# Kernel optimization log

Hardware: AMD Instinct MI355X
Metric: run time of the kernel (lower is better)

The kernel has to match this reference:

```python
import jax, jax.numpy as jnp
import numpy as np
from jax import lax

N_USERS, N_ITEMS = 40000, 60000
N = N_USERS + N_ITEMS
D = 64
E = 800000
L = 2
BIAS = 1e-4
AUTO_T = 1.0


def setup_inputs() -> dict:
    key = jax.random.key(0)
    ks = jax.random.split(key, 12)
    emb0 = jax.random.normal(ks[0], (N, D), dtype=jnp.float32) * 0.1
    h_idx = jax.random.randint(ks[1], (E,), 0, N)
    t_idx = jax.random.randint(ks[2], (E,), 0, N)
    # symmetric normalization G = D^-1/2 A D^-1/2 (values share A's sparsity)
    deg = jax.ops.segment_sum(jnp.ones((E,), jnp.float32), h_idx, num_segments=N)
    dis = jnp.where(deg > 0, deg ** -0.5, 0.0)
    G_values = dis[h_idx] * dis[t_idx]
    # Gumbel noise: -log(-log(U(bias, 1-bias)))
    ue = jax.random.uniform(ks[3], (L, E), minval=BIAS, maxval=1.0 - BIAS)
    edge_gumbel = -jnp.log(-jnp.log(ue))
    un = jax.random.uniform(ks[4], (L, N, D), minval=BIAS, maxval=1.0 - BIAS)
    emb_gumbel = -jnp.log(-jnp.log(un))
    sc2, sc1 = (2.0 / (3 * D)) ** 0.5, (2.0 / (2 * D)) ** 0.5
    edge_W1 = jax.random.normal(ks[5], (L, 2 * D, D), dtype=jnp.float32) * sc2
    edge_b1 = jnp.zeros((L, D), jnp.float32)
    edge_W2 = jax.random.normal(ks[6], (L, D, 1), dtype=jnp.float32) * sc1
    edge_b2 = jnp.zeros((L, 1), jnp.float32)
    emb_W1 = jax.random.normal(ks[7], (L, D, D), dtype=jnp.float32) * sc1
    emb_b1 = jnp.zeros((L, D), jnp.float32)
    emb_W2 = jax.random.normal(ks[8], (L, D, D), dtype=jnp.float32) * sc1
    emb_b2 = jnp.zeros((L, D), jnp.float32)
    return dict(emb0=emb0, h_idx=h_idx, t_idx=t_idx, G_values=G_values,
                edge_gumbel=edge_gumbel, emb_gumbel=emb_gumbel,
                edge_W1=edge_W1, edge_b1=edge_b1, edge_W2=edge_W2, edge_b2=edge_b2,
                emb_W1=emb_W1, emb_b1=emb_b1, emb_W2=emb_W2, emb_b2=emb_b2)


def _spmm(vals, h, t, x, n):
    # out[h] += vals * x[t]
    return jax.ops.segment_sum(vals[:, None] * x[t], h, num_segments=n)


def reference(emb0, h_idx, t_idx, G_values, edge_gumbel, emb_gumbel,
              edge_W1, edge_b1, edge_W2, edge_b2,
              emb_W1, emb_b1, emb_W2, emb_b2):
    n = emb0.shape[0]
    e0 = e1 = e2 = emb0
    s0 = s1 = s2 = emb0
    for i in range(edge_W1.shape[0]):
        # branch 0: plain normalized propagation
        gnn0 = _spmm(G_values, h_idx, t_idx, e0, n)
        # branch 1: learned edge reweighting (auto_augment_s, is_norm=True)
        edge_emb = jnp.concatenate([e1[h_idx], e1[t_idx]], axis=1)      # [E, 2D]
        logits = jnp.maximum(edge_emb @ edge_W1[i] + edge_b1[i], 0.0) @ edge_W2[i] + edge_b2[i]  # [E,1]
        w = jax.nn.sigmoid((edge_gumbel[i][:, None] + logits) / AUTO_T)[:, 0]
        w = lax.stop_gradient(w)                                         # detached in original
        row = jax.ops.segment_sum(w, h_idx, num_segments=n)
        dinv = jnp.where(row > 0, 1.0 / row, 0.0)                        # pow(-1).nan_to_num(0)
        vals1 = dinv[h_idx] * w
        gnn1 = _spmm(vals1, h_idx, t_idx, e1, n)
        # branch 2: learned feature gating (auto_augment_f)
        lg = jnp.maximum(e2 @ emb_W1[i] + emb_b1[i], 0.0) @ emb_W2[i] + emb_b2[i]
        gate = lax.stop_gradient(jax.nn.sigmoid((emb_gumbel[i] + lg) / AUTO_T))
        gnn2 = _spmm(G_values, h_idx, t_idx, gate * e2, n)
        e0 = gnn0 + e0
        e1 = gnn1 + e1
        e2 = gnn2 + e2
        s0 = s0 + e0
        s1 = s1 + e1
        s2 = s2 + e2
    return jnp.stack([s0, s1, s2])  # [3, N, D]; split rows into users/items downstream
```

## Files before the change

### kernel.cpp

```cpp
#include <hip/hip_runtime.h>
#include <hip/hip_bf16.h>
#include <math.h>

#define PK_STRIDE 256
#define LDA 72

typedef float v4f __attribute__((ext_vector_type(4)));
typedef __attribute__((ext_vector_type(8))) short s8;
typedef __attribute__((ext_vector_type(4))) float f4;

__device__ __forceinline__ float4 f4z() { return make_float4(0.f, 0.f, 0.f, 0.f); }
__device__ __forceinline__ void fma4(float4& a, float s, const float4& v) {
  a.x = fmaf(s, v.x, a.x); a.y = fmaf(s, v.y, a.y);
  a.z = fmaf(s, v.z, a.z); a.w = fmaf(s, v.w, a.w);
}
__device__ __forceinline__ float4 add4(const float4& a, const float4& b) {
  return make_float4(a.x + b.x, a.y + b.y, a.z + b.z, a.w + b.w);
}
__device__ __forceinline__ void stnt4(float* p, const float4& v) {
  v4f u; u.x = v.x; u.y = v.y; u.z = v.z; u.w = v.w;
  __builtin_nontemporal_store(u, (v4f*)p);
}
__device__ __forceinline__ float4 lo4(const uint4& u) {
  float4 f;
  f.x = __uint_as_float(u.x << 16);
  f.y = __uint_as_float(u.x & 0xffff0000u);
  f.z = __uint_as_float(u.y << 16);
  f.w = __uint_as_float(u.y & 0xffff0000u);
  return f;
}
__device__ __forceinline__ float4 hi4(const uint4& u) {
  float4 f;
  f.x = __uint_as_float(u.z << 16);
  f.y = __uint_as_float(u.z & 0xffff0000u);
  f.z = __uint_as_float(u.w << 16);
  f.w = __uint_as_float(u.w & 0xffff0000u);
  return f;
}
__device__ __forceinline__ float4 cvt2(const uint2& u) {
  float4 f;
  f.x = __uint_as_float(u.x << 16);
  f.y = __uint_as_float(u.x & 0xffff0000u);
  f.z = __uint_as_float(u.y << 16);
  f.w = __uint_as_float(u.y & 0xffff0000u);
  return f;
}
__device__ __forceinline__ float4 ldbf4(const unsigned short* p) {
  ushort4 u = *(const ushort4*)p;
  float4 f;
  f.x = __uint_as_float((unsigned)u.x << 16);
  f.y = __uint_as_float((unsigned)u.y << 16);
  f.z = __uint_as_float((unsigned)u.z << 16);
  f.w = __uint_as_float((unsigned)u.w << 16);
  return f;
}
__device__ __forceinline__ unsigned short f2bf(float v) {
  __hip_bfloat16 h = __float2bfloat16(v);
  return *reinterpret_cast<unsigned short*>(&h);
}
__device__ __forceinline__ unsigned pack2(float a, float b) {
  return ((unsigned)f2bf(b) << 16) | (unsigned)f2bf(a);
}
__device__ __forceinline__ void st4bf(unsigned short* p, const float4& v) {
  ushort4 u;
  u.x = f2bf(v.x); u.y = f2bf(v.y); u.z = f2bf(v.z); u.w = f2bf(v.w);
  *(ushort4*)p = u;
}
__device__ __forceinline__ float fsig(float x) {
  return __builtin_amdgcn_rcpf(1.f + __expf(-x));
}

__global__ void hist_k(const int* __restrict__ h, int* __restrict__ deg, int E) {
  int i = blockIdx.x * blockDim.x + threadIdx.x;
  if (i < E) atomicAdd(&deg[h[i]], 1);
}

__global__ void scanA_k(const int* __restrict__ deg, int* __restrict__ rp,
                        int* __restrict__ sums, int N) {
  __shared__ int s[1024];
  int i = blockIdx.x * 1024 + threadIdx.x;
  int v = (i < N) ? deg[i] : 0;
  s[threadIdx.x] = v;
  __syncthreads();
  for (int off = 1; off < 1024; off <<= 1) {
    int t = (threadIdx.x >= (unsigned)off) ? s[threadIdx.x - off] : 0;
    __syncthreads();
    s[threadIdx.x] += t;
    __syncthreads();
  }
  if (i < N) rp[i] = s[threadIdx.x] - v;
  if (threadIdx.x == 1023) sums[blockIdx.x] = s[1023];
}

__global__ void scanB_k(int* sums, int nch) {
  int lane = threadIdx.x;
  int run = 0;
  for (int base = 0; base < nch; base += 64) {
    int v = (base + lane < nch) ? sums[base + lane] : 0;
    int incl = v;
    for (int off = 1; off < 64; off <<= 1) {
      int t = __shfl_up(incl, off, 64);
      if (lane >= off) incl += t;
    }
    if (base + lane < nch) sums[base + lane] = run + (incl - v);
    run += __shfl(incl, 63, 64);
  }
}

__global__ void scanC_k(int* __restrict__ rp, int* __restrict__ cur,
                        const int* __restrict__ sums, int N, int E) {
  int i = blockIdx.x * blockDim.x + threadIdx.x;
  if (i < N) {
    int v = rp[i] + sums[i >> 10];
    rp[i] = v; cur[i] = v;
  } else if (i == N) {
    rp[N] = E;
  }
}

__global__ void fill_k(const int* __restrict__ h, const int* __restrict__ t_idx,
                       const float* __restrict__ G, const float* __restrict__ gum,
                       int* __restrict__ cur, int4* __restrict__ emeta,
                       float* __restrict__ cgum, int E, int L) {
  int i = blockIdx.x * blockDim.x + threadIdx.x;
  if (i < E) {
    int pos = atomicAdd(&cur[h[i]], 1);
    int4 em;
    em.x = t_idx[i] * PK_STRIDE;
    em.y = __float_as_int(G[i]);
    em.z = __float_as_int(gum[i]);
    em.w = (L > 1) ? __float_as_int(gum[(size_t)E + i]) : 0;
    emeta[pos] = em;
    if (L > 2)
      for (int l = 2; l < L; l++) cgum[(size_t)l * E + pos] = gum[(size_t)l * E + i];
  }
}

__global__ void wprep_k(const float* __restrict__ edge_W1,
                        const float* __restrict__ emb_W1,
                        const float* __restrict__ emb_W2,
                        unsigned short* __restrict__ wxT,
                        unsigned short* __restrict__ w1T,
                        unsigned short* __restrict__ w2T, int L) {
  const int per = 128 * 64 + 64 * 64 + 64 * 64;
  int i = blockIdx.x * blockDim.x + threadIdx.x;
  if (i >= L * per) return;
  int layer = i / per, r = i % per;
  if (r < 8192) {
    int j = r >> 6, k = r & 63;
    float v = (j < 64) ? edge_W1[((size_t)layer * 128 + k) * 64 + j]
                       : edge_W1[((size_t)layer * 128 + 64 + k) * 64 + (j - 64)];
    wxT[(size_t)layer * 8192 + j * 64 + k] = f2bf(v);
  } else if (r < 8192 + 4096) {
    int q = r - 8192; int n = q >> 6, k = q & 63;
    w1T[(size_t)layer * 4096 + n * 64 + k] =
        f2bf(emb_W1[((size_t)layer * 64 + k) * 64 + n]);
  } else {
    int q = r - 12288; int n = q >> 6, k = q & 63;
    w2T[(size_t)layer * 4096 + n * 64 + k] =
        f2bf(emb_W2[((size_t)layer * 64 + k) * 64 + n]);
  }
}

template <int FIRST>
__global__ __launch_bounds__(256) void dense_k(
    const float* __restrict__ emb0,
    const unsigned short* __restrict__ pkin,
    const unsigned short* __restrict__ e2b,
    const unsigned short* __restrict__ wxT,
    const unsigned short* __restrict__ w1T,
    const unsigned short* __restrict__ w2T,
    const float* __restrict__ b1,
    const float* __restrict__ b2,
    const float* __restrict__ gum,
    unsigned short* __restrict__ xhb,
    unsigned short* __restrict__ pk,
    unsigned short* __restrict__ emb0b,
    int N) {
  __shared__ unsigned short a1[64 * LDA];
  __shared__ unsigned short a2[64 * LDA];
  int tid = threadIdx.x;
  int n0 = blockIdx.x * 64;
  if (FIRST) {
    for (int i = tid; i < 64 * 8; i += 256) {
      int r = i >> 3, c8 = (i & 7) * 8;
      uint4 u = make_uint4(0, 0, 0, 0);
      if (n0 + r < N) {
        const float* src = emb0 + (size_t)(n0 + r) * 64 + c8;
        float4 lo = *(const float4*)src;
        float4 hi = *(const float4*)(src + 4);
        u.x = pack2(lo.x, lo.y); u.y = pack2(lo.z, lo.w);
        u.z = pack2(hi.x, hi.y); u.w = pack2(hi.z, hi.w);
        *(uint4*)(emb0b + (size_t)(n0 + r) * 64 + c8) = u;
      }
      *(uint4*)(a1 + r * LDA + c8) = u;
      *(uint4*)(a2 + r * LDA + c8) = u;
    }
  } else {
    for (int i = tid; i < 64 * 16; i += 256) {
      int r = i >> 4, c = i & 15;
      ushort4 v1 = make_ushort4(0, 0, 0, 0), v2 = v1;
      if (n0 + r < N) {
        v1 = *(const ushort4*)(pkin + (size_t)(n0 + r) * PK_STRIDE + c * 8 + 4);
        v2 = *(const ushort4*)(e2b + (size_t)(n0 + r) * 64 + c * 4);
      }
      *(ushort4*)(a1 + r * LDA + c * 4) = v1;
      *(ushort4*)(a2 + r * LDA + c * 4) = v2;
    }
  }
  __syncthreads();
  int wv = tid >> 6, l = tid & 63;
  int l15 = l & 15, lg = l >> 4;
  int wr = wv * 16;
  int arow = wr + l15;
  s8 af1_0 = *(const s8*)(a1 + arow * LDA + 8 * lg);
  s8 af1_1 = *(const s8*)(a1 + arow * LDA + 32 + 8 * lg);
#pragma unroll
  for (int ct = 0; ct < 8; ct++) {
    f4 acc = {0.f, 0.f, 0.f, 0.f};
    s8 b0 = *(const s8*)(wxT + (ct * 16 + l15) * 64 + 8 * lg);
    s8 bI = *(const s8*)(wxT + (ct * 16 + l15) * 64 + 32 + 8 * lg);
    acc = __builtin_amdgcn_mfma_f32_16x16x32_bf16(af1_0, b0, acc, 0, 0, 0);
    acc = __builtin_amdgcn_mfma_f32_16x16x32_bf16(af1_1, bI, acc, 0, 0, 0);
#pragma unroll
    for (int j = 0; j < 4; j++) {
      int n = n0 + wr + lg * 4 + j;
      if (n < N) {
        if (ct < 4) {
          xhb[(size_t)n * 64 + ct * 16 + l15] = f2bf(acc[j]);
        } else {
          int c2 = (ct - 4) * 16 + l15;
          pk[(size_t)n * PK_STRIDE + 128 + (c2 >> 2) * 8 + 4 + (c2 & 3)] = f2bf(acc[j]);
        }
      }
    }
  }
  s8 af2_0 = *(const s8*)(a2 + arow * LDA + 8 * lg);
  s8 af2_1 = *(const s8*)(a2 + arow * LDA + 32 + 8 * lg);
#pragma unroll
  for (int ct = 0; ct < 4; ct++) {
    f4 acc = {0.f, 0.f, 0.f, 0.f};
    s8 b0 = *(const s8*)(w1T + (ct * 16 + l15) * 64 + 8 * lg);
    s8 bI = *(const s8*)(w1T + (ct * 16 + l15) * 64 + 32 + 8 * lg);
    acc = __builtin_amdgcn_mfma_f32_16x16x32_bf16(af2_0, b0, acc, 0, 0, 0);
    acc = __builtin_amdgcn_mfma_f32_16x16x32_bf16(af2_1, bI, acc, 0, 0, 0);
    float bb = b1[ct * 16 + l15];
#pragma unroll
    for (int j = 0; j < 4; j++) {
      float h = fmaxf(acc[j] + bb, 0.f);
      a1[(wr + lg * 4 + j) * LDA + ct * 16 + l15] = f2bf(h);
    }
  }
  s8 afh_0 = *(const s8*)(a1 + arow * LDA + 8 * lg);
  s8 afh_1 = *(const s8*)(a1 + arow * LDA + 32 + 8 * lg);
#pragma unroll
  for (int ct = 0; ct < 4; ct++) {
    f4 acc = {0.f, 0.f, 0.f, 0.f};
    s8 b0 = *(const s8*)(w2T + (ct * 16 + l15) * 64 + 8 * lg);
    s8 bI = *(const s8*)(w2T + (ct * 16 + l15) * 64 + 32 + 8 * lg);
    acc = __builtin_amdgcn_mfma_f32_16x16x32_bf16(afh_0, b0, acc, 0, 0, 0);
    acc = __builtin_amdgcn_mfma_f32_16x16x32_bf16(afh_1, bI, acc, 0, 0, 0);
    int c2 = ct * 16 + l15;
    float bb = b2[c2];
#pragma unroll
    for (int j = 0; j < 4; j++) {
      int row = wr + lg * 4 + j;
      int n = n0 + row;
      if (n < N) {
        float gv = gum[(size_t)n * 64 + c2];
        float e2v = __uint_as_float((unsigned)a2[row * LDA + c2] << 16);
        float y = e2v * fsig(gv + acc[j] + bb);
        pk[(size_t)n * PK_STRIDE + 128 + (c2 >> 2) * 8 + (c2 & 3)] = f2bf(y);
      }
    }
  }
}

#define CH 2

#define LOADCH(Abuf, Bbuf, I0)                                          \
  _Pragma("unroll")                                                     \
  for (int c = 0; c < CH; c++) {                                        \
    int i_ = (I0) + c;                                                  \
    int tof_ = __shfl(em.x, i_ & 15, 16);                               \
    if (i_ < cnt) {                                                     \
      const unsigned short* pr_ = pk + (size_t)tof_ + l * 8;            \
      Abuf[c] = *(const uint4*)(pr_);                                   \
      Bbuf[c] = *(const uint4*)(pr_ + 128);                             \
    }                                                                   \
  }

#define COMPCH(Abuf, Bbuf, I0)                                          \
  _Pragma("unroll")                                                     \
  for (int c = 0; c < CH; c++) {                                        \
    int i_ = (I0) + c;                                                  \
    float gg_ = __shfl(__int_as_float(em.y), i_ & 15, 16);              \
    float gu_ = __shfl(guv, i_ & 15, 16);                               \
    if (i_ < cnt) {                                                     \
      float4 v0_ = lo4(Abuf[c]);                                        \
      float4 v1_ = hi4(Abuf[c]);                                        \
      float4 vy_ = lo4(Bbuf[c]);                                        \
      float4 xt_ = hi4(Bbuf[c]);                                        \
      float pq_ = fmaxf(xb1.x + xt_.x, 0.f) * w2v.x                     \
                + fmaxf(xb1.y + xt_.y, 0.f) * w2v.y                     \
                + fmaxf(xb1.z + xt_.z, 0.f) * w2v.z                     \
                + fmaxf(xb1.w + xt_.w, 0.f) * w2v.w;                    \
      pq_ += __shfl_xor(pq_, 1, 16);                                    \
      pq_ += __shfl_xor(pq_, 2, 16);                                    \
      pq_ += __shfl_xor(pq_, 4, 16);                                    \
      pq_ += __shfl_xor(pq_, 8, 16);                                    \
      float w_ = fsig(gu_ + pq_ + b2s);                                 \
      wsum += w_;                                                       \
      fma4(acc0, gg_, v0_);                                             \
      fma4(acc1, w_, v1_);                                              \
      fma4(acc2, gg_, vy_);                                             \
    }                                                                   \
  }

#define LOADCH_F(Abuf, Bbuf, I0)                                        \
  _Pragma("unroll")                                                     \
  for (int c = 0; c < CH; c++) {                                        \
    int i_ = (I0) + c;                                                  \
    int tof_ = __shfl(em.x, i_ & 15, 16);                               \
    if (i_ < cnt) {                                                     \
      Abuf[c] = *(const uint2*)(emb0b + (size_t)(tof_ >> 2) + l * 4);   \
      Bbuf[c] = *(const uint4*)(pk + (size_t)tof_ + 128 + l * 8);       \
    }                                                                   \
  }

#define COMPCH_F(Abuf, Bbuf, I0)                                        \
  _Pragma("unroll")                                                     \
  for (int c = 0; c < CH; c++) {                                        \
    int i_ = (I0) + c;                                                  \
    float gg_ = __shfl(__int_as_float(em.y), i_ & 15, 16);              \
    float gu_ = __shfl(guv, i_ & 15, 16);                               \
    if (i_ < cnt) {                                                     \
      float4 v0_ = cvt2(Abuf[c]);                                       \
      float4 vy_ = lo4(Bbuf[c]);                                        \
      float4 xt_ = hi4(Bbuf[c]);                                        \
      float pq_ = fmaxf(xb1.x + xt_.x, 0.f) * w2v.x                     \
                + fmaxf(xb1.y + xt_.y, 0.f) * w2v.y                     \
                + fmaxf(xb1.z + xt_.z, 0.f) * w2v.z                     \
                + fmaxf(xb1.w + xt_.w, 0.f) * w2v.w;                    \
      pq_ += __shfl_xor(pq_, 1, 16);                                    \
      pq_ += __shfl_xor(pq_, 2, 16);                                    \
      pq_ += __shfl_xor(pq_, 4, 16);                                    \
      pq_ += __shfl_xor(pq_, 8, 16);                                    \
      float w_ = fsig(gu_ + pq_ + b2s);                                 \
      wsum += w_;                                                       \
      fma4(acc0, gg_, v0_);                                             \
      fma4(acc1, w_, v0_);                                              \
      fma4(acc2, gg_, vy_);                                             \
    }                                                                   \
  }

template <int FIRST, int OUTM, int GSEL>
__global__ __launch_bounds__(256) void spmm3f_k(const int* __restrict__ rp,
    const int4* __restrict__ emeta, const float* __restrict__ cgum,
    const unsigned short* __restrict__ pk, const unsigned short* __restrict__ xhb,
    const unsigned short* __restrict__ e2b_in,
    const unsigned short* __restrict__ emb0b,
    const float* __restrict__ b1, const float* __restrict__ W2,
    const float* __restrict__ b2,
    unsigned short* __restrict__ pkn, unsigned short* __restrict__ e2b,
    float* __restrict__ out0, float* __restrict__ out1, float* __restrict__ out2,
    int N) {
  int g = threadIdx.x >> 4;
  int l = threadIdx.x & 15;
  int n = blockIdx.x * 16 + g;
  if (n >= N) return;
  int jb = rp[n], je = rp[n + 1];
  size_t o64 = (size_t)n * 64 + l * 4;
  float4 xh4 = ldbf4(xhb + o64);
  float4 b1v = *(const float4*)(b1 + l * 4);
  float4 xb1 = add4(xh4, b1v);
  float4 w2v = *(const float4*)(W2 + l * 4);
  float b2s = b2[0];
  float4 rc0, rc1, rc2;
  if (FIRST) {
    rc0 = ldbf4(emb0b + o64);
    rc1 = rc0; rc2 = rc0;
  } else {
    uint4 rA = *(const uint4*)(pk + (size_t)n * PK_STRIDE + l * 8);
    rc0 = lo4(rA);
    rc1 = hi4(rA);
    rc2 = ldbf4(e2b_in + o64);
  }
  float4 acc0 = f4z(), acc1 = f4z(), acc2 = f4z();
  float wsum = 0.f;
  for (int base = jb; base < je; base += 16) {
    int idx = base + l;
    bool valid = idx < je;
    int4 em = valid ? emeta[idx] : make_int4(0, 0, 0, 0);
    float guv;
    if (GSEL == 0) guv = __int_as_float(em.z);
    else if (GSEL == 1) guv = __int_as_float(em.w);
    else guv = valid ? cgum[idx] : 0.f;
    int cnt = min(16, je - base);
    if (FIRST) {
      uint2 A0[CH], A1[CH];
      uint4 B0[CH], B1[CH];
      LOADCH_F(A0, B0, 0)
      for (int i0 = 0; i0 < cnt; i0 += 2 * CH) {
        LOADCH_F(A1, B1, i0 + CH)
        COMPCH_F(A0, B0, i0)
        LOADCH_F(A0, B0, i0 + 2 * CH)
        COMPCH_F(A1, B1, i0 + CH)
      }
    } else {
      uint4 A0[CH], B0[CH], A1[CH], B1[CH];
      LOADCH(A0, B0, 0)
      for (int i0 = 0; i0 < cnt; i0 += 2 * CH) {
        LOADCH(A1, B1, i0 + CH)
        COMPCH(A0, B0, i0)
        LOADCH(A0, B0, i0 + 2 * CH)
        COMPCH(A1, B1, i0 + CH)
      }
    }
  }
  float dinv = (wsum > 0.f) ? __builtin_amdgcn_rcpf(wsum) : 0.f;
  float4 en0 = add4(acc0, rc0);
  acc1.x *= dinv; acc1.y *= dinv; acc1.z *= dinv; acc1.w *= dinv;
  float4 en1 = add4(acc1, rc1);
  float4 en2 = add4(acc2, rc2);
  if (OUTM != 1) {
    uint4 wA;
    wA.x = pack2(en0.x, en0.y); wA.y = pack2(en0.z, en0.w);
    wA.z = pack2(en1.x, en1.y); wA.w = pack2(en1.z, en1.w);
    *(uint4*)(pkn + (size_t)n * PK_STRIDE + l * 8) = wA;
    st4bf(e2b + o64, en2);
  }
  if (OUTM == 1) {
    float4 base = ldbf4(emb0b + o64);
    stnt4(out0 + o64, add4(base, add4(rc0, en0)));
    stnt4(out1 + o64, add4(base, add4(rc1, en1)));
    stnt4(out2 + o64, add4(base, add4(rc2, en2)));
  } else if (OUTM == 2) {
    *(float4*)(out0 + o64) = add4(rc0, en0);
    *(float4*)(out1 + o64) = add4(rc1, en1);
    *(float4*)(out2 + o64) = add4(rc2, en2);
  } else if (OUTM == 3) {
    *(float4*)(out0 + o64) = add4(*(const float4*)(out0 + o64), en0);
    *(float4*)(out1 + o64) = add4(*(const float4*)(out1 + o64), en1);
    *(float4*)(out2 + o64) = add4(*(const float4*)(out2 + o64), en2);
  }
}

extern "C" void kernel_launch(void* const* d_in, const int* in_sizes, int n_in,
                              void* d_out, int out_size, void* d_ws, size_t ws_size,
                              hipStream_t stream) {
  const float* emb0        = (const float*)d_in[0];
  const int*   h_idx       = (const int*)d_in[1];
  const int*   t_idx       = (const int*)d_in[2];
  const float* G_values    = (const float*)d_in[3];
  const float* edge_gumbel = (const float*)d_in[4];
  const float* emb_gumbel  = (const float*)d_in[5];
  const float* edge_W1     = (const float*)d_in[6];
  const float* edge_b1     = (const float*)d_in[7];
  const float* edge_W2     = (const float*)d_in[8];
  const float* edge_b2     = (const float*)d_in[9];
  const float* emb_W1      = (const float*)d_in[10];
  const float* emb_b1      = (const float*)d_in[11];
  const float* emb_W2      = (const float*)d_in[12];
  const float* emb_b2      = (const float*)d_in[13];

  const int D = 64;
  const int N = in_sizes[0] / D;
  const int E = in_sizes[1];
  const int L = in_sizes[4] / E;
  const size_t ND = (size_t)N * D;

  char* p = (char*)d_ws;
  auto alloc = [&](size_t bytes) -> char* {
    char* r = p;
    p += (bytes + 255) & ~(size_t)255;
    return r;
  };
  unsigned short* xhb   = (unsigned short*)alloc(ND * 2);
  unsigned short* e2b   = (unsigned short*)alloc(ND * 2);
  unsigned short* emb0b = (unsigned short*)alloc(ND * 2);
  unsigned short* pkA   = (unsigned short*)alloc((size_t)N * PK_STRIDE * 2);
  unsigned short* pkB   = (unsigned short*)alloc((size_t)N * PK_STRIDE * 2);
  int4*  emeta = (int4*)alloc((size_t)E * 16);
  float* cgum  = (float*)alloc((L > 2 ? (size_t)L * E : 1) * 4);
  unsigned short* wxT = (unsigned short*)alloc((size_t)L * 8192 * 2);
  unsigned short* w1T = (unsigned short*)alloc((size_t)L * 4096 * 2);
  unsigned short* w2T = (unsigned short*)alloc((size_t)L * 4096 * 2);
  int*   deg   = (int*)alloc((size_t)N * 4);
  int*   cur   = (int*)alloc((size_t)N * 4);
  int*   rp    = (int*)alloc(((size_t)N + 1) * 4);
  int*   sums  = (int*)alloc(1024 * 4);

  float* out = (float*)d_out;

  hipMemsetAsync(deg, 0, (size_t)N * 4, stream);
  hist_k<<<(E + 255) / 256, 256, 0, stream>>>(h_idx, deg, E);
  int nch = (N + 1023) / 1024;
  scanA_k<<<nch, 1024, 0, stream>>>(deg, rp, sums, N);
  scanB_k<<<1, 64, 0, stream>>>(sums, nch);
  scanC_k<<<(N + 256) / 256, 256, 0, stream>>>(rp, cur, sums, N, E);
  fill_k<<<(E + 255) / 256, 256, 0, stream>>>(h_idx, t_idx, G_values, edge_gumbel,
                                              cur, emeta, cgum, E, L);
  wprep_k<<<(L * 16384 + 255) / 256, 256, 0, stream>>>(edge_W1, emb_W1, emb_W2,
                                                       wxT, w1T, w2T, L);

  int nb64 = (N + 63) / 64;
  int nb16 = (N + 15) / 16;

  for (int i = 0; i < L; i++) {
    unsigned short* pkc = (i & 1) ? pkB : pkA;
    unsigned short* pkn = (i & 1) ? pkA : pkB;
    if (i == 0)
      dense_k<1><<<nb64, 256, 0, stream>>>(emb0, pkc, e2b,
                                           wxT, w1T, w2T,
                                           emb_b1, emb_b2, emb_gumbel,
                                           xhb, pkc, emb0b, N);
    else
      dense_k<0><<<nb64, 256, 0, stream>>>(emb0, pkc, e2b,
                                           wxT + (size_t)i * 8192,
                                           w1T + (size_t)i * 4096,
                                           w2T + (size_t)i * 4096,
                                           emb_b1 + (size_t)i * 64,
                                           emb_b2 + (size_t)i * 64,
                                           emb_gumbel + (size_t)i * ND,
                                           xhb, pkc, emb0b, N);
    const float* eb1 = edge_b1 + (size_t)i * 64;
    const float* eW2 = edge_W2 + (size_t)i * 64;
    const float* eb2 = edge_b2 + i;
    if (L == 2) {
      if (i == 0)
        spmm3f_k<1, 0, 0><<<nb16, 256, 0, stream>>>(rp, emeta, cgum, pkc, xhb, e2b,
                                                    emb0b, eb1, eW2, eb2,
                                                    pkn, e2b,
                                                    out, out + ND, out + 2 * ND, N);
      else
        spmm3f_k<0, 1, 1><<<nb16, 256, 0, stream>>>(rp, emeta, cgum, pkc, xhb, e2b,
                                                    emb0b, eb1, eW2, eb2,
                                                    pkn, e2b,
                                                    out, out + ND, out + 2 * ND, N);
    } else {
      const float* cgl = (L > 2) ? cgum + (size_t)i * E : cgum;
      if (i == 0)
        spmm3f_k<1, 2, 0><<<nb16, 256, 0, stream>>>(rp, emeta, cgl, pkc, xhb, e2b,
                                                    emb0b, eb1, eW2, eb2,
                                                    pkn, e2b,
                                                    out, out + ND, out + 2 * ND, N);
      else if (i == 1)
        spmm3f_k<0, 3, 1><<<nb16, 256, 0, stream>>>(rp, emeta, cgl, pkc, xhb, e2b,
                                                    emb0b, eb1, eW2, eb2,
                                                    pkn, e2b,
                                                    out, out + ND, out + 2 * ND, N);
      else
        spmm3f_k<0, 3, 2><<<nb16, 256, 0, stream>>>(rp, emeta, cgl, pkc, xhb, e2b,
                                                    emb0b, eb1, eW2, eb2,
                                                    pkn, e2b,
                                                    out, out + ND, out + 2 * ND, N);
    }
  }
}
```

Measured before the change: 333.4 us.

## Fuse CSR preprocessing kernels into one cooperative kernel with grid syncs

Replaces the memset, histogram, three-pass scan, fill and weight-prep launches with a single cooperative kernel of 1024 blocks that separates the phases with grid-wide syncs. The scan now uses 256-element chunks with wave shuffles in place of a shared-memory Hillis-Steele scan. The goal is to cut launch overhead and inter-kernel gaps in the preprocessing chain. In exchange it adds grid.sync costs, and the grid-stride loops run with less parallelism than the old one-thread-per-element launches.

After: 807.4 us. 142% more time.

```diff
diff --git a/kernel.cpp b/kernel.cpp
--- a/kernel.cpp
+++ b/kernel.cpp
@@ -1,6 +1,9 @@
 #include <hip/hip_runtime.h>
+#include <hip/hip_cooperative_groups.h>
 #include <hip/hip_bf16.h>
 #include <math.h>
+
+namespace cg = cooperative_groups;
 
 #define PK_STRIDE 256
 #define LDA 72
@@ -70,60 +73,88 @@
   return __builtin_amdgcn_rcpf(1.f + __expf(-x));
 }
 
-__global__ void hist_k(const int* __restrict__ h, int* __restrict__ deg, int E) {
-  int i = blockIdx.x * blockDim.x + threadIdx.x;
-  if (i < E) atomicAdd(&deg[h[i]], 1);
-}
-
-__global__ void scanA_k(const int* __restrict__ deg, int* __restrict__ rp,
-                        int* __restrict__ sums, int N) {
-  __shared__ int s[1024];
-  int i = blockIdx.x * 1024 + threadIdx.x;
-  int v = (i < N) ? deg[i] : 0;
-  s[threadIdx.x] = v;
-  __syncthreads();
-  for (int off = 1; off < 1024; off <<= 1) {
-    int t = (threadIdx.x >= (unsigned)off) ? s[threadIdx.x - off] : 0;
+__global__ void prep_k(const int* __restrict__ h, const int* __restrict__ t_idx,
+                       const float* __restrict__ G, const float* __restrict__ gum,
+                       const float* __restrict__ edge_W1,
+                       const float* __restrict__ emb_W1,
+                       const float* __restrict__ emb_W2,
+                       unsigned short* __restrict__ wxT,
+                       unsigned short* __restrict__ w1T,
+                       unsigned short* __restrict__ w2T,
+                       int* __restrict__ deg, int* __restrict__ rp,
+                       int* __restrict__ cur, int* __restrict__ csum,
+                       int4* __restrict__ emeta, float* __restrict__ cgum,
+                       int N, int E, int L) {
+  cg::grid_group grid = cg::this_grid();
+  __shared__ int wsumS[4];
+  int gtid = blockIdx.x * blockDim.x + threadIdx.x;
+  int gsz = gridDim.x * blockDim.x;
+  for (int i = gtid; i < N; i += gsz) deg[i] = 0;
+  const int per = 16384;
+  for (int i = gtid; i < L * per; i += gsz) {
+    int layer = i / per, r = i % per;
+    if (r < 8192) {
+      int j = r >> 6, k = r & 63;
+      float v = (j < 64) ? edge_W1[((size_t)layer * 128 + k) * 64 + j]
+                         : edge_W1[((size_t)layer * 128 + 64 + k) * 64 + (j - 64)];
+      wxT[(size_t)layer * 8192 + j * 64 + k] = f2bf(v);
+    } else if (r < 12288) {
+      int q = r - 8192; int n = q >> 6, k = q & 63;
+      w1T[(size_t)layer * 4096 + n * 64 + k] =
+          f2bf(emb_W1[((size_t)layer * 64 + k) * 64 + n]);
+    } else {
+      int q = r - 12288; int n = q >> 6, k = q & 63;
+      w2T[(size_t)layer * 4096 + n * 64 + k] =
+          f2bf(emb_W2[((size_t)layer * 64 + k) * 64 + n]);
+    }
+  }
+  grid.sync();
+  for (int i = gtid; i < E; i += gsz) atomicAdd(&deg[h[i]], 1);
+  grid.sync();
+  int nch = (N + 255) >> 8;
+  for (int c = blockIdx.x; c < nch; c += gridDim.x) {
+    int i = (c << 8) + threadIdx.x;
+    int v = (i < N) ? deg[i] : 0;
+    int lane = threadIdx.x & 63, wid = threadIdx.x >> 6;
+    int incl = v;
+#pragma unroll
+    for (int off = 1; off < 64; off <<= 1) {
+      int tt = __shfl_up(incl, off, 64);
+      if (lane >= off) incl += tt;
+    }
+    if (lane == 63) wsumS[wid] = incl;
     __syncthreads();
-    s[threadIdx.x] += t;
+    int add = 0;
+    for (int w = 0; w < wid; w++) add += wsumS[w];
+    incl += add;
+    if (i < N) rp[i] = incl - v;
+    if (threadIdx.x == 255) csum[c] = incl;
     __syncthreads();
   }
-  if (i < N) rp[i] = s[threadIdx.x] - v;
-  if (threadIdx.x == 1023) sums[blockIdx.x] = s[1023];
-}
-
-__global__ void scanB_k(int* sums, int nch) {
-  int lane = threadIdx.x;
-  int run = 0;
-  for (int base = 0; base < nch; base += 64) {
-    int v = (base + lane < nch) ? sums[base + lane] : 0;
-    int incl = v;
-    for (int off = 1; off < 64; off <<= 1) {
-      int t = __shfl_up(incl, off, 64);
-      if (lane >= off) incl += t;
-    }
-    if (base + lane < nch) sums[base + lane] = run + (incl - v);
-    run += __shfl(incl, 63, 64);
-  }
-}
-
-__global__ void scanC_k(int* __restrict__ rp, int* __restrict__ cur,
-                        const int* __restrict__ sums, int N, int E) {
-  int i = blockIdx.x * blockDim.x + threadIdx.x;
-  if (i < N) {
-    int v = rp[i] + sums[i >> 10];
+  grid.sync();
+  if (blockIdx.x == 0 && threadIdx.x < 64) {
+    int lane = threadIdx.x;
+    int run = 0;
+    for (int base = 0; base < nch; base += 64) {
+      int v = (base + lane < nch) ? csum[base + lane] : 0;
+      int incl = v;
+#pragma unroll
+      for (int off = 1; off < 64; off <<= 1) {
+        int tt = __shfl_up(incl, off, 64);
+        if (lane >= off) incl += tt;
+      }
+      if (base + lane < nch) csum[base + lane] = run + (incl - v);
+      run += __shfl(incl, 63, 64);
+    }
+  }
+  grid.sync();
+  for (int i = gtid; i < N; i += gsz) {
+    int v = rp[i] + csum[i >> 8];
     rp[i] = v; cur[i] = v;
-  } else if (i == N) {
-    rp[N] = E;
-  }
-}
-
-__global__ void fill_k(const int* __restrict__ h, const int* __restrict__ t_idx,
-                       const float* __restrict__ G, const float* __restrict__ gum,
-                       int* __restrict__ cur, int4* __restrict__ emeta,
-                       float* __restrict__ cgum, int E, int L) {
-  int i = blockIdx.x * blockDim.x + threadIdx.x;
-  if (i < E) {
+  }
+  if (gtid == 0) rp[N] = E;
+  grid.sync();
+  for (int i = gtid; i < E; i += gsz) {
     int pos = atomicAdd(&cur[h[i]], 1);
     int4 em;
     em.x = t_idx[i] * PK_STRIDE;
@@ -133,32 +164,6 @@
     emeta[pos] = em;
     if (L > 2)
       for (int l = 2; l < L; l++) cgum[(size_t)l * E + pos] = gum[(size_t)l * E + i];
-  }
-}
-
-__global__ void wprep_k(const float* __restrict__ edge_W1,
-                        const float* __restrict__ emb_W1,
-                        const float* __restrict__ emb_W2,
-                        unsigned short* __restrict__ wxT,
-                        unsigned short* __restrict__ w1T,
-                        unsigned short* __restrict__ w2T, int L) {
-  const int per = 128 * 64 + 64 * 64 + 64 * 64;
-  int i = blockIdx.x * blockDim.x + threadIdx.x;
-  if (i >= L * per) return;
-  int layer = i / per, r = i % per;
-  if (r < 8192) {
-    int j = r >> 6, k = r & 63;
-    float v = (j < 64) ? edge_W1[((size_t)layer * 128 + k) * 64 + j]
-                       : edge_W1[((size_t)layer * 128 + 64 + k) * 64 + (j - 64)];
-    wxT[(size_t)layer * 8192 + j * 64 + k] = f2bf(v);
-  } else if (r < 8192 + 4096) {
-    int q = r - 8192; int n = q >> 6, k = q & 63;
-    w1T[(size_t)layer * 4096 + n * 64 + k] =
-        f2bf(emb_W1[((size_t)layer * 64 + k) * 64 + n]);
-  } else {
-    int q = r - 12288; int n = q >> 6, k = q & 63;
-    w2T[(size_t)layer * 4096 + n * 64 + k] =
-        f2bf(emb_W2[((size_t)layer * 64 + k) * 64 + n]);
   }
 }
 
@@ -465,9 +470,9 @@
   const float* emb_b2      = (const float*)d_in[13];
 
   const int D = 64;
-  const int N = in_sizes[0] / D;
-  const int E = in_sizes[1];
-  const int L = in_sizes[4] / E;
+  int N = in_sizes[0] / D;
+  int E = in_sizes[1];
+  int L = in_sizes[4] / E;
   const size_t ND = (size_t)N * D;
 
   char* p = (char*)d_ws;
@@ -489,20 +494,22 @@
   int*   deg   = (int*)alloc((size_t)N * 4);
   int*   cur   = (int*)alloc((size_t)N * 4);
   int*   rp    = (int*)alloc(((size_t)N + 1) * 4);
-  int*   sums  = (int*)alloc(1024 * 4);
+  int*   csum  = (int*)alloc(2048 * 4);
 
   float* out = (float*)d_out;
 
-  hipMemsetAsync(deg, 0, (size_t)N * 4, stream);
-  hist_k<<<(E + 255) / 256, 256, 0, stream>>>(h_idx, deg, E);
-  int nch = (N + 1023) / 1024;
-  scanA_k<<<nch, 1024, 0, stream>>>(deg, rp, sums, N);
-  scanB_k<<<1, 64, 0, stream>>>(sums, nch);
-  scanC_k<<<(N + 256) / 256, 256, 0, stream>>>(rp, cur, sums, N, E);
-  fill_k<<<(E + 255) / 256, 256, 0, stream>>>(h_idx, t_idx, G_values, edge_gumbel,
-                                              cur, emeta, cgum, E, L);
-  wprep_k<<<(L * 16384 + 255) / 256, 256, 0, stream>>>(edge_W1, emb_W1, emb_W2,
-                                                       wxT, w1T, w2T, L);
+  {
+    void* args[] = {
+      (void*)&h_idx, (void*)&t_idx, (void*)&G_values, (void*)&edge_gumbel,
+      (void*)&edge_W1, (void*)&emb_W1, (void*)&emb_W2,
+      (void*)&wxT, (void*)&w1T, (void*)&w2T,
+      (void*)&deg, (void*)&rp, (void*)&cur, (void*)&csum,
+      (void*)&emeta, (void*)&cgum,
+      (void*)&N, (void*)&E, (void*)&L
+    };
+    hipLaunchCooperativeKernel((const void*)prep_k, dim3(1024), dim3(256),
+                               args, 0, stream);
+  }
 
   int nb64 = (N + 63) / 64;
   int nb16 = (N + 15) / 16;
```

## Stage dense-kernel outputs in LDS for coalesced stores; fold weight prep into histogram

Applied to the files above, without the earlier changes.

The dense kernel now writes its MFMA results (the xh projection and the packed gate and edge-projection rows) into shared-memory staging tiles first. After a barrier it copies them out as coalesced 16-byte row stores, replacing scattered 2-byte global writes. The separate weight-transpose kernel is merged into the histogram kernel, which becomes a fixed-size grid-stride launch, removing one launch. The cost is about 26 KB of extra LDS per block, which may lower occupancy, plus one extra barrier.

Result: no change. 333.5 us (+0.1%).

```diff
diff --git a/kernel.cpp b/kernel.cpp
--- a/kernel.cpp
+++ b/kernel.cpp
@@ -4,6 +4,8 @@
 
 #define PK_STRIDE 256
 #define LDA 72
+#define STY 136
+#define STX 72
 
 typedef float v4f __attribute__((ext_vector_type(4)));
 typedef __attribute__((ext_vector_type(8))) short s8;
@@ -70,9 +72,34 @@
   return __builtin_amdgcn_rcpf(1.f + __expf(-x));
 }
 
-__global__ void hist_k(const int* __restrict__ h, int* __restrict__ deg, int E) {
-  int i = blockIdx.x * blockDim.x + threadIdx.x;
-  if (i < E) atomicAdd(&deg[h[i]], 1);
+__global__ void hist_k(const int* __restrict__ h, int* __restrict__ deg, int E,
+                       const float* __restrict__ edge_W1,
+                       const float* __restrict__ emb_W1,
+                       const float* __restrict__ emb_W2,
+                       unsigned short* __restrict__ wxT,
+                       unsigned short* __restrict__ w1T,
+                       unsigned short* __restrict__ w2T, int L) {
+  int gtid = blockIdx.x * blockDim.x + threadIdx.x;
+  int gsz = gridDim.x * blockDim.x;
+  for (int i = gtid; i < E; i += gsz) atomicAdd(&deg[h[i]], 1);
+  const int per = 16384;
+  for (int i = gtid; i < L * per; i += gsz) {
+    int layer = i / per, r = i % per;
+    if (r < 8192) {
+      int j = r >> 6, k = r & 63;
+      float v = (j < 64) ? edge_W1[((size_t)layer * 128 + k) * 64 + j]
+                         : edge_W1[((size_t)layer * 128 + 64 + k) * 64 + (j - 64)];
+      wxT[(size_t)layer * 8192 + j * 64 + k] = f2bf(v);
+    } else if (r < 12288) {
+      int q = r - 8192; int n = q >> 6, k = q & 63;
+      w1T[(size_t)layer * 4096 + n * 64 + k] =
+          f2bf(emb_W1[((size_t)layer * 64 + k) * 64 + n]);
+    } else {
+      int q = r - 12288; int n = q >> 6, k = q & 63;
+      w2T[(size_t)layer * 4096 + n * 64 + k] =
+          f2bf(emb_W2[((size_t)layer * 64 + k) * 64 + n]);
+    }
+  }
 }
 
 __global__ void scanA_k(const int* __restrict__ deg, int* __restrict__ rp,
@@ -133,32 +160,6 @@
     emeta[pos] = em;
     if (L > 2)
       for (int l = 2; l < L; l++) cgum[(size_t)l * E + pos] = gum[(size_t)l * E + i];
-  }
-}
-
-__global__ void wprep_k(const float* __restrict__ edge_W1,
-                        const float* __restrict__ emb_W1,
-                        const float* __restrict__ emb_W2,
-                        unsigned short* __restrict__ wxT,
-                        unsigned short* __restrict__ w1T,
-                        unsigned short* __restrict__ w2T, int L) {
-  const int per = 128 * 64 + 64 * 64 + 64 * 64;
-  int i = blockIdx.x * blockDim.x + threadIdx.x;
-  if (i >= L * per) return;
-  int layer = i / per, r = i % per;
-  if (r < 8192) {
-    int j = r >> 6, k = r & 63;
-    float v = (j < 64) ? edge_W1[((size_t)layer * 128 + k) * 64 + j]
-                       : edge_W1[((size_t)layer * 128 + 64 + k) * 64 + (j - 64)];
-    wxT[(size_t)layer * 8192 + j * 64 + k] = f2bf(v);
-  } else if (r < 8192 + 4096) {
-    int q = r - 8192; int n = q >> 6, k = q & 63;
-    w1T[(size_t)layer * 4096 + n * 64 + k] =
-        f2bf(emb_W1[((size_t)layer * 64 + k) * 64 + n]);
-  } else {
-    int q = r - 12288; int n = q >> 6, k = q & 63;
-    w2T[(size_t)layer * 4096 + n * 64 + k] =
-        f2bf(emb_W2[((size_t)layer * 64 + k) * 64 + n]);
   }
 }
 
@@ -179,6 +180,8 @@
     int N) {
   __shared__ unsigned short a1[64 * LDA];
   __shared__ unsigned short a2[64 * LDA];
+  __shared__ unsigned short stgY[64 * STY];
+  __shared__ unsigned short stgX[64 * STX];
   int tid = threadIdx.x;
   int n0 = blockIdx.x * 64;
   if (FIRST) {
@@ -224,14 +227,12 @@
     acc = __builtin_amdgcn_mfma_f32_16x16x32_bf16(af1_1, bI, acc, 0, 0, 0);
 #pragma unroll
     for (int j = 0; j < 4; j++) {
-      int n = n0 + wr + lg * 4 + j;
-      if (n < N) {
-        if (ct < 4) {
-          xhb[(size_t)n * 64 + ct * 16 + l15] = f2bf(acc[j]);
-        } else {
-          int c2 = (ct - 4) * 16 + l15;
-          pk[(size_t)n * PK_STRIDE + 128 + (c2 >> 2) * 8 + 4 + (c2 & 3)] = f2bf(acc[j]);
-        }
+      int row = wr + lg * 4 + j;
+      if (ct < 4) {
+        stgX[row * STX + ct * 16 + l15] = f2bf(acc[j]);
+      } else {
+        int c2 = (ct - 4) * 16 + l15;
+        stgY[row * STY + (c2 >> 2) * 8 + 4 + (c2 & 3)] = f2bf(acc[j]);
       }
     }
   }
@@ -266,13 +267,22 @@
     for (int j = 0; j < 4; j++) {
       int row = wr + lg * 4 + j;
       int n = n0 + row;
-      if (n < N) {
-        float gv = gum[(size_t)n * 64 + c2];
-        float e2v = __uint_as_float((unsigned)a2[row * LDA + c2] << 16);
-        float y = e2v * fsig(gv + acc[j] + bb);
-        pk[(size_t)n * PK_STRIDE + 128 + (c2 >> 2) * 8 + (c2 & 3)] = f2bf(y);
-      }
-    }
+      float gv = (n < N) ? gum[(size_t)n * 64 + c2] : 0.f;
+      float e2v = __uint_as_float((unsigned)a2[row * LDA + c2] << 16);
+      float y = e2v * fsig(gv + acc[j] + bb);
+      stgY[row * STY + (c2 >> 2) * 8 + (c2 & 3)] = f2bf(y);
+    }
+  }
+  __syncthreads();
+  for (int i = tid; i < 64 * 16; i += 256) {
+    int r = i >> 4, c = i & 15;
+    uint4 v = *(const uint4*)(stgY + r * STY + c * 8);
+    if (n0 + r < N) *(uint4*)(pk + (size_t)(n0 + r) * PK_STRIDE + 128 + c * 8) = v;
+  }
+  for (int i = tid; i < 64 * 8; i += 256) {
+    int r = i >> 3, c = i & 7;
+    uint4 v = *(const uint4*)(stgX + r * STX + c * 8);
+    if (n0 + r < N) *(uint4*)(xhb + (size_t)(n0 + r) * 64 + c * 8) = v;
   }
 }
 
@@ -494,15 +504,14 @@
   float* out = (float*)d_out;
 
   hipMemsetAsync(deg, 0, (size_t)N * 4, stream);
-  hist_k<<<(E + 255) / 256, 256, 0, stream>>>(h_idx, deg, E);
+  hist_k<<<1024, 256, 0, stream>>>(h_idx, deg, E, edge_W1, emb_W1, emb_W2,
+                                   wxT, w1T, w2T, L);
   int nch = (N + 1023) / 1024;
   scanA_k<<<nch, 1024, 0, stream>>>(deg, rp, sums, N);
   scanB_k<<<1, 64, 0, stream>>>(sums, nch);
   scanC_k<<<(N + 256) / 256, 256, 0, stream>>>(rp, cur, sums, N, E);
   fill_k<<<(E + 255) / 256, 256, 0, stream>>>(h_idx, t_idx, G_values, edge_gumbel,
                                               cur, emeta, cgum, E, L);
-  wprep_k<<<(L * 16384 + 255) / 256, 256, 0, stream>>>(edge_W1, emb_W1, emb_W2,
-                                                       wxT, w1T, w2T, L);
 
   int nb64 = (N + 63) / 64;
   int nb16 = (N + 15) / 16;
```
